# Kernel optimization log

Hardware: AMD Instinct MI355X
Metric: run time of the kernel (lower is better)

Reference implementation:

```python
import jax, jax.numpy as jnp
import numpy as np

B, C, L = 32, 8, 2048
K, S = 512, 64  # num_shapelets, shapelets_size


def setup_inputs() -> dict:
    key = jax.random.key(0)
    k1, k2 = jax.random.split(key)
    x = jax.random.normal(k1, (B, C, L), dtype=jnp.float32)
    shapelets = jax.random.normal(k2, (C, K, S), dtype=jnp.float32)
    return {"x": x, "shapelets": shapelets}


def reference(x, shapelets):
    # x: [B, C, L]; shapelets: [C, K, S]
    s = shapelets.shape[-1]
    n_dims = x.shape[1]
    W = x.shape[2] - s + 1  # number of sliding windows
    # unfold(2, S, 1): gather overlapping windows -> [B, C, W, S]
    idx = jnp.arange(W)[:, None] + jnp.arange(s)[None, :]
    xw = x[:, :, idx]
    # L2-normalize windows along window length (clamp min like torch)
    xw = xw / jnp.maximum(jnp.linalg.norm(xw, axis=-1, keepdims=True), 1e-8)
    # L2-normalize shapelets along length
    sn = shapelets / jnp.maximum(jnp.linalg.norm(shapelets, axis=-1, keepdims=True), 1e-8)
    # matmul [B,C,W,S] @ [C,S,K] then sum over C, fused into one einsum -> [B, W, K]
    sim = jnp.einsum('bcws,cks->bwk', xw, sn) / n_dims
    sim = jax.nn.relu(sim)
    # max over window positions -> [B, K]; keep the singleton channel dim like torch ([B,1,K])
    out = jnp.max(sim, axis=1)
    return out[:, None, :]
```

## Files before the change

kernel.cpp:

```cpp
#include <hip/hip_runtime.h>


#define B_ 32
#define C_ 8
#define L_ 2048
#define K_ 512
#define S_ 64
#define W_ 1985
#define TW 128

typedef _Float16 f16x8 __attribute__((ext_vector_type(8)));
typedef float f32x16 __attribute__((ext_vector_type(16)));
typedef float f32x4u __attribute__((ext_vector_type(4), aligned(4)));

__global__ __launch_bounds__(256)
void prep_k(const float* __restrict__ x, const float* __restrict__ sh,
            _Float16* __restrict__ Bp, float* __restrict__ invn,
            float* __restrict__ out) {
    __shared__ float xr[L_];
    const int tid = threadIdx.x;
    const int blk = blockIdx.x;

    if (blk < 128) {
        const int sb   = blk * 4 + (tid >> 6);
        const int c    = sb >> 6;
        const int kq   = (sb >> 4) & 3;
        const int nt   = sb & 15;
        const int lane = tid & 63;
        const int half = lane >> 5;
        const int q    = nt * 32 + (lane & 31);

        const float4* sp = (const float4*)(sh + (size_t)(c * K_ + q) * S_);
        float ss = 0.f;
        #pragma unroll
        for (int i = 0; i < 8; ++i) {
            float4 v = sp[half * 8 + i];
            ss += v.x * v.x + v.y * v.y + v.z * v.z + v.w * v.w;
        }
        ss += __shfl_xor(ss, 32);
        float inv = 1.f / fmaxf(sqrtf(ss), 1e-8f);

        float4 u0 = sp[kq * 4 + half * 2];
        float4 u1 = sp[kq * 4 + half * 2 + 1];
        f16x8 o;
        o[0] = (_Float16)(u0.x * inv); o[1] = (_Float16)(u0.y * inv);
        o[2] = (_Float16)(u0.z * inv); o[3] = (_Float16)(u0.w * inv);
        o[4] = (_Float16)(u1.x * inv); o[5] = (_Float16)(u1.y * inv);
        o[6] = (_Float16)(u1.z * inv); o[7] = (_Float16)(u1.w * inv);
        ((f16x8*)Bp)[((c * 4 + kq) * 16 + nt) * 64 + lane] = o;
    } else {
        const int r = blk - 128;
        const float* xp = x + (size_t)r * L_;
        for (int i = tid; i < L_ / 4; i += 256)
            ((float4*)xr)[i] = ((const float4*)xp)[i];
        __syncthreads();

        float* ivp = invn + (size_t)r * L_;
        const int w0 = tid * 8;
        float ss = 0.f;
        if (w0 < W_) {
            #pragma unroll
            for (int j = 0; j < S_; ++j) { float v = xr[w0 + j]; ss += v * v; }
        }
        #pragma unroll
        for (int u = 0; u < 8; ++u) {
            int w = w0 + u;
            float o = 0.f;
            if (u > 0 && w < W_)
                ss += xr[w + 63] * xr[w + 63] - xr[w - 1] * xr[w - 1];
            if (w < W_) o = 0.125f / fmaxf(sqrtf(ss), 1e-8f);
            if (w < L_) ivp[w] = o;
        }
        if (r < 64) out[r * 256 + tid] = 0.f;
    }
}

__global__ __launch_bounds__(256, 2)
void mcs_k(const float* __restrict__ x, const _Float16* __restrict__ Bp,
           const float* __restrict__ invn, float* __restrict__ out) {
    const int wt  = blockIdx.x;
    const int ng  = blockIdx.y;
    const int b   = blockIdx.z;
    const int tid = threadIdx.x;
    const int lane = tid & 63;
    const int wv   = tid >> 6;
    const int mg   = wv >> 1;
    const int nw   = wv & 1;

    const int l31 = lane & 31;
    const int lh  = lane >> 5;
    const int Wb  = wt * TW + mg * 64;
    const int m0  = Wb + l31;
    const int m1  = Wb + 32 + l31;

    f32x16 acc[2][4];
    #pragma unroll
    for (int mt = 0; mt < 2; ++mt)
        #pragma unroll
        for (int nt = 0; nt < 4; ++nt)
            #pragma unroll
            for (int r = 0; r < 16; ++r) acc[mt][nt][r] = 0.f;

    #pragma unroll 1
    for (int c = 0; c < C_; ++c) {
        const float* ivp  = invn + (size_t)(b * C_ + c) * L_;
        const float* xrow = x + (size_t)(b * C_ + c) * L_;
        float iv0 = ivp[m0];
        float iv1 = ivp[m1];

        const f16x8* bbase = (const f16x8*)Bp +
            ((c * 4) * 16 + ng * 8 + nw * 4) * 64 + lane;
        f16x8 bfr[4][4];
        #pragma unroll
        for (int ks = 0; ks < 4; ++ks)
            #pragma unroll
            for (int nt = 0; nt < 4; ++nt)
                bfr[ks][nt] = bbase[(ks * 16 + nt) * 64];

        f16x8 af[2][4];
        #pragma unroll
        for (int mt = 0; mt < 2; ++mt) {
            float iv = mt ? iv1 : iv0;
            #pragma unroll
            for (int ks = 0; ks < 4; ++ks) {
                int p  = Wb + mt * 32 + l31 + ks * 16 + lh * 8;
                int pc = p <= L_ - 8 ? p : L_ - 8;
                f32x4u v0 = *(const f32x4u*)(xrow + pc);
                f32x4u v1 = *(const f32x4u*)(xrow + pc + 4);
                f16x8 o;
                o[0] = (_Float16)(v0[0] * iv); o[1] = (_Float16)(v0[1] * iv);
                o[2] = (_Float16)(v0[2] * iv); o[3] = (_Float16)(v0[3] * iv);
                o[4] = (_Float16)(v1[0] * iv); o[5] = (_Float16)(v1[1] * iv);
                o[6] = (_Float16)(v1[2] * iv); o[7] = (_Float16)(v1[3] * iv);
                af[mt][ks] = o;
            }
        }

        #pragma unroll
        for (int ks = 0; ks < 4; ++ks)
            #pragma unroll
            for (int nt = 0; nt < 4; ++nt)
                #pragma unroll
                for (int mt = 0; mt < 2; ++mt)
                    acc[mt][nt] = __builtin_amdgcn_mfma_f32_32x32x16_f16(
                        af[mt][ks], bfr[ks][nt], acc[mt][nt], 0, 0, 0);
    }

    #pragma unroll
    for (int nt = 0; nt < 4; ++nt) {
        float m = 0.f;
        #pragma unroll
        for (int mt = 0; mt < 2; ++mt)
            #pragma unroll
            for (int r = 0; r < 16; ++r)
                m = fmaxf(m, acc[mt][nt][r]);
        m = fmaxf(m, __shfl_xor(m, 32));
        if (lane < 32)
            atomicMax((unsigned int*)(out + b * K_ + ng * 256 + nw * 128 + nt * 32 + l31),
                      __float_as_uint(m));
    }
}

extern "C" void kernel_launch(void* const* d_in, const int* in_sizes, int n_in,
                              void* d_out, int out_size, void* d_ws, size_t ws_size,
                              hipStream_t stream) {
    const float* x  = (const float*)d_in[0];
    const float* sh = (const float*)d_in[1];
    float* out = (float*)d_out;
    _Float16* Bp  = (_Float16*)d_ws;
    float* invn   = (float*)((char*)d_ws + (size_t)K_ * 512 * sizeof(_Float16));

    prep_k<<<dim3(384), dim3(256), 0, stream>>>(x, sh, Bp, invn, out);
    mcs_k<<<dim3(16, 2, B_), dim3(256), 0, stream>>>(x, Bp, invn, out);
}
```

Baseline: 99.53 us.

## Software-pipeline A/B register fragment loads across k-steps in MFMA loop

Replaces the per-channel loop, which loaded all B and A fragments and then issued the MFMAs, with a fully unrolled 32-step loop over (channel, k-slice). B fragments are prefetched two steps ahead in a triple buffer, and raw x values and inverse norms one step ahead in double buffers. The aim is to hide global-load latency behind MFMA work instead of stalling at the top of each channel. Full unrolling may raise register pressure and code size, which could hurt occupancy under launch_bounds(256,2).

```diff
diff --git a/kernel.cpp b/kernel.cpp
--- a/kernel.cpp
+++ b/kernel.cpp
@@ -90,8 +90,39 @@
     const int l31 = lane & 31;
     const int lh  = lane >> 5;
     const int Wb  = wt * TW + mg * 64;
-    const int m0  = Wb + l31;
-    const int m1  = Wb + 32 + l31;
+
+    const float* xbase  = x    + (size_t)(b * C_) * L_;
+    const float* ivbase = invn + (size_t)(b * C_) * L_;
+    const f16x8* Bq     = (const f16x8*)Bp;
+    const int coloff    = (ng * 8 + nw * 4) * 64 + lane;
+
+    f16x8  Bbuf[3][4];
+    f32x4u Abuf[2][4];
+    float  iv0b[2], iv1b[2];
+
+    auto issueB = [&](int s, int slot) {
+        const int c = s >> 2, ks = s & 3;
+        const f16x8* bb = Bq + ((c * 4 + ks) * 16) * 64 + coloff;
+        #pragma unroll
+        for (int nt = 0; nt < 4; ++nt) Bbuf[slot][nt] = bb[nt * 64];
+    };
+    auto issueA = [&](int s, int slot) {
+        const int c = s >> 2, ks = s & 3;
+        const float* xr = xbase + c * L_;
+        #pragma unroll
+        for (int mt = 0; mt < 2; ++mt) {
+            int p  = Wb + mt * 32 + l31 + ks * 16 + lh * 8;
+            int pc = p <= L_ - 8 ? p : L_ - 8;
+            Abuf[slot][mt * 2]     = *(const f32x4u*)(xr + pc);
+            Abuf[slot][mt * 2 + 1] = *(const f32x4u*)(xr + pc + 4);
+        }
+    };
+
+    iv0b[0] = ivbase[Wb + l31];
+    iv1b[0] = ivbase[Wb + 32 + l31];
+    issueB(0, 0);
+    issueA(0, 0);
+    issueB(1, 1);
 
     f32x16 acc[2][4];
     #pragma unroll
@@ -101,49 +132,37 @@
             #pragma unroll
             for (int r = 0; r < 16; ++r) acc[mt][nt][r] = 0.f;
 
-    #pragma unroll 1
-    for (int c = 0; c < C_; ++c) {
-        const float* ivp  = invn + (size_t)(b * C_ + c) * L_;
-        const float* xrow = x + (size_t)(b * C_ + c) * L_;
-        float iv0 = ivp[m0];
-        float iv1 = ivp[m1];
-
-        const f16x8* bbase = (const f16x8*)Bp +
-            ((c * 4) * 16 + ng * 8 + nw * 4) * 64 + lane;
-        f16x8 bfr[4][4];
+    #pragma unroll
+    for (int s = 0; s < 32; ++s) {
+        const int c = s >> 2, ks = s & 3;
+        if (s + 2 < 32) issueB(s + 2, (s + 2) % 3);
+        if (s + 1 < 32) issueA(s + 1, (s + 1) & 1);
+        if (ks == 0 && c + 1 < C_) {
+            const float* ivr = ivbase + (c + 1) * L_;
+            iv0b[(c + 1) & 1] = ivr[Wb + l31];
+            iv1b[(c + 1) & 1] = ivr[Wb + 32 + l31];
+        }
+        const float iv0 = iv0b[c & 1], iv1 = iv1b[c & 1];
+        f16x8 af0, af1;
+        {
+            f32x4u v0 = Abuf[s & 1][0], v1 = Abuf[s & 1][1];
+            af0[0] = (_Float16)(v0[0] * iv0); af0[1] = (_Float16)(v0[1] * iv0);
+            af0[2] = (_Float16)(v0[2] * iv0); af0[3] = (_Float16)(v0[3] * iv0);
+            af0[4] = (_Float16)(v1[0] * iv0); af0[5] = (_Float16)(v1[1] * iv0);
+            af0[6] = (_Float16)(v1[2] * iv0); af0[7] = (_Float16)(v1[3] * iv0);
+            f32x4u w0 = Abuf[s & 1][2], w1 = Abuf[s & 1][3];
+            af1[0] = (_Float16)(w0[0] * iv1); af1[1] = (_Float16)(w0[1] * iv1);
+            af1[2] = (_Float16)(w0[2] * iv1); af1[3] = (_Float16)(w0[3] * iv1);
+            af1[4] = (_Float16)(w1[0] * iv1); af1[5] = (_Float16)(w1[1] * iv1);
+            af1[6] = (_Float16)(w1[2] * iv1); af1[7] = (_Float16)(w1[3] * iv1);
+        }
         #pragma unroll
-        for (int ks = 0; ks < 4; ++ks)
-            #pragma unroll
-            for (int nt = 0; nt < 4; ++nt)
-                bfr[ks][nt] = bbase[(ks * 16 + nt) * 64];
-
-        f16x8 af[2][4];
-        #pragma unroll
-        for (int mt = 0; mt < 2; ++mt) {
-            float iv = mt ? iv1 : iv0;
-            #pragma unroll
-            for (int ks = 0; ks < 4; ++ks) {
-                int p  = Wb + mt * 32 + l31 + ks * 16 + lh * 8;
-                int pc = p <= L_ - 8 ? p : L_ - 8;
-                f32x4u v0 = *(const f32x4u*)(xrow + pc);
-                f32x4u v1 = *(const f32x4u*)(xrow + pc + 4);
-                f16x8 o;
-                o[0] = (_Float16)(v0[0] * iv); o[1] = (_Float16)(v0[1] * iv);
-                o[2] = (_Float16)(v0[2] * iv); o[3] = (_Float16)(v0[3] * iv);
-                o[4] = (_Float16)(v1[0] * iv); o[5] = (_Float16)(v1[1] * iv);
-                o[6] = (_Float16)(v1[2] * iv); o[7] = (_Float16)(v1[3] * iv);
-                af[mt][ks] = o;
-            }
+        for (int nt = 0; nt < 4; ++nt) {
+            acc[0][nt] = __builtin_amdgcn_mfma_f32_32x32x16_f16(
+                af0, Bbuf[s % 3][nt], acc[0][nt], 0, 0, 0);
+            acc[1][nt] = __builtin_amdgcn_mfma_f32_32x32x16_f16(
+                af1, Bbuf[s % 3][nt], acc[1][nt], 0, 0, 0);
         }
-
-        #pragma unroll
-        for (int ks = 0; ks < 4; ++ks)
-            #pragma unroll
-            for (int nt = 0; nt < 4; ++nt)
-                #pragma unroll
-                for (int mt = 0; mt < 2; ++mt)
-                    acc[mt][nt] = __builtin_amdgcn_mfma_f32_32x32x16_f16(
-                        af[mt][ks], bfr[ks][nt], acc[mt][nt], 0, 0, 0);
     }
 
     #pragma unroll
```

After: 103.7 us. +4.1%, slower.
